# Performance work log

Hardware: AMD Instinct MI355X
Metric: run time of the kernel (lower is better)

Reference implementation:

```python
import jax, jax.numpy as jnp
import numpy as np

B, H, V, L, M, D, C = 64, 512, 50000, 400, 128, 64, 64
HC = 2 * D + M + 4  # controller LSTM hidden size (one head)
EPS = 1e-8


def _lstm_step(x, h, c, Wih, Whh, bih, bhh):
    g = x @ Wih.T + bih + h @ Whh.T + bhh
    i, f, gg, o = jnp.split(g, 4, axis=-1)
    c2 = jax.nn.sigmoid(f) * c + jax.nn.sigmoid(i) * jnp.tanh(gg)
    return jax.nn.sigmoid(o) * jnp.tanh(c2), c2


def _head_params(hc):
    # slices exactly as in LSTMMemoryController (k=0, single head)
    keys = hc[:, :M]                               # [B, M]
    kstr = jnp.exp(hc[:, D:D + 1])                 # [B, 1]
    gate = jax.nn.sigmoid(hc[:, D + 1:D + 2])      # [B, 1]
    erase = jax.nn.sigmoid(hc[:, D + 4:M + D + 4]) # [B, M]
    add = jax.nn.sigmoid(hc[:, 2 * D + 4:M + 2 * D + 4])  # [B, M]
    return keys, kstr, gate, erase, add


def _addressing(keys, kstr, gate, heads, memory):
    # torch cosine_similarity(keys.unsqueeze(2), memory, dim=2):
    # keys [B,M] broadcast along memory_dim D
    num = keys * memory.sum(-1)                                   # [B, M]
    nk = jnp.maximum(jnp.abs(keys) * jnp.sqrt(jnp.float32(D)), EPS)
    nm = jnp.maximum(jnp.linalg.norm(memory, axis=-1), EPS)
    cos = num / (nk * nm)
    content = jax.nn.softmax(kstr * cos, axis=1)                  # [B, M]
    # faithful to original: heads[k] indexes axis 0 (k=0) -> shape [1, M]
    gated = gate * content + (1.0 - gate) * heads[0]
    return gated[:, None, :]                                      # [B, 1, M]


def reference(input_ids, h0, c0, encoder_outputs, word_occurrence_indicator,
              coverage, memory, read_heads, write_heads,
              read_h, read_c, write_h, write_c,
              emb, attn_W, attn_b, cov_W, state_W, comb_W, comb_b,
              rpre_W, rpre_b, wpre_W, wpre_b,
              r_Wih, r_Whh, r_bih, r_bhh,
              w_Wih, w_Whh, w_bih, w_bhh,
              l_Wih, l_Whh, l_bih, l_bhh,
              out_W, out_b):
    embedded = emb[input_ids]                                     # [B, H]
    ia = jnp.concatenate([embedded, h0], 1) @ attn_W.T + attn_b  # [B, L]
    tc = (coverage + ia) @ cov_W.T
    ts = c0 @ state_W.T
    aw = jax.nn.softmax(tc + ia + ts, axis=1)                     # [B, L]
    attn_applied = jnp.einsum('bl,blh->bh', aw, encoder_outputs)  # [B, H]
    out0 = jnp.concatenate([embedded, attn_applied], 1) @ comb_W.T + comb_b  # [B, H]

    hm = jnp.concatenate([h0, memory.reshape(-1, M * D)], 1)
    rh, rc = _lstm_step(hm @ rpre_W.T + rpre_b, read_h, read_c, r_Wih, r_Whh, r_bih, r_bhh)
    wh, wc = _lstm_step(hm @ wpre_W.T + wpre_b, write_h, write_c, w_Wih, w_Whh, w_bih, w_bhh)
    rk, rks, rg, _, _ = _head_params(rh)
    wk, wks, wg, we, wa = _head_params(wh)
    rw = _addressing(rk, rks, rg, read_heads, memory)             # [B, 1, M]
    ww = _addressing(wk, wks, wg, write_heads, memory)            # [B, 1, M]

    read_in = jnp.einsum('bkm,bmd->bkd', rw, memory).reshape(-1, D)
    h1, c1 = _lstm_step(jnp.concatenate([out0, read_in], 1), h0, c0,
                        l_Wih, l_Whh, l_bih, l_bhh)
    # residual (h1 + out0) is computed in the original but unused by its output path

    w0 = ww[:, 0, :, None]                                        # [B, M, 1]
    new_memory = memory * (1.0 - w0 * we[:, :, None]) + w0 * wa[:, :, None]
    new_coverage = coverage + ia

    log_probs = jax.nn.log_softmax(c1[:, None, :] @ out_W.T + out_b, axis=-1)  # [B, 1, V]
    return log_probs, h1, c1, new_memory, new_coverage


def setup_inputs() -> dict:
    key = jax.random.key(0)
    ks = iter(jax.random.split(key, 48))

    def rn(shape, fan_in):
        return jax.random.normal(next(ks), shape, jnp.float32) / np.sqrt(fan_in)

    inp = {
        'input_ids': jax.random.randint(next(ks), (B,), 0, V),
        'h0': jax.random.normal(next(ks), (B, H), jnp.float32),
        'c0': jax.random.normal(next(ks), (B, H), jnp.float32),
        'encoder_outputs': jax.random.normal(next(ks), (B, L, H), jnp.float32),
        'word_occurrence_indicator': jnp.zeros((B, L), jnp.float32),
        'coverage': jnp.zeros((B, L), jnp.float32),
        'memory': jax.random.normal(next(ks), (B, M, D), jnp.float32),
        'read_heads': jnp.zeros((B, 1, M), jnp.float32),
        'write_heads': jnp.zeros((B, 1, M), jnp.float32),
        'read_h': jnp.zeros((B, HC), jnp.float32),
        'read_c': jnp.zeros((B, HC), jnp.float32),
        'write_h': jnp.zeros((B, HC), jnp.float32),
        'write_c': jnp.zeros((B, HC), jnp.float32),
        'emb': rn((V, H), H),
        'attn_W': rn((L, 2 * H), 2 * H), 'attn_b': jnp.zeros((L,), jnp.float32),
        'cov_W': rn((L, L), L),
        'state_W': rn((L, H), H),
        'comb_W': rn((H, 2 * H), 2 * H), 'comb_b': jnp.zeros((H,), jnp.float32),
        'rpre_W': rn((C, M * D + H), M * D + H), 'rpre_b': jnp.zeros((C,), jnp.float32),
        'wpre_W': rn((C, M * D + H), M * D + H), 'wpre_b': jnp.zeros((C,), jnp.float32),
        'r_Wih': rn((4 * HC, C), C), 'r_Whh': rn((4 * HC, HC), HC),
        'r_bih': jnp.zeros((4 * HC,), jnp.float32), 'r_bhh': jnp.zeros((4 * HC,), jnp.float32),
        'w_Wih': rn((4 * HC, C), C), 'w_Whh': rn((4 * HC, HC), HC),
        'w_bih': jnp.zeros((4 * HC,), jnp.float32), 'w_bhh': jnp.zeros((4 * HC,), jnp.float32),
        'l_Wih': rn((4 * H, H + D), H + D), 'l_Whh': rn((4 * H, H), H),
        'l_bih': jnp.zeros((4 * H,), jnp.float32), 'l_bhh': jnp.zeros((4 * H,), jnp.float32),
        'out_W': rn((V, H), H), 'out_b': jnp.zeros((V,), jnp.float32),
    }
    return inp
```

## Files before the change

### kernel.cpp

```cpp
#include <hip/hip_runtime.h>
#include <math.h>

#define BB 64
#define HH 512
#define VV 50000
#define LL 400
#define MM 128
#define DD 64
#define HC 260
#define EPSF 1e-8f

__device__ __forceinline__ float sigmoidf(float x){ return 1.0f/(1.0f+expf(-x)); }
__device__ __forceinline__ float wave_max(float v){
  #pragma unroll
  for(int o=32;o;o>>=1) v = fmaxf(v, __shfl_xor(v,o));
  return v;
}
__device__ __forceinline__ float wave_sum(float v){
  #pragma unroll
  for(int o=32;o;o>>=1) v += __shfl_xor(v,o);
  return v;
}

__global__ void k_embed(const int* __restrict__ ids, const float* __restrict__ emb,
                        const float* __restrict__ h0, float* __restrict__ xcat1,
                        float* __restrict__ xcat2){
  int idx = blockIdx.x*256 + threadIdx.x;
  if (idx >= BB*HH) return;
  int b = idx >> 9, h = idx & 511;
  float e = emb[(long)ids[b]*HH + h];
  xcat1[b*1024 + h] = e;
  xcat2[b*1024 + h] = e;
  xcat1[b*1024 + 512 + h] = h0[idx];
}

template<int NB, int FUSE>
__global__ __launch_bounds__(256) void k_gemv(const float* __restrict__ A,
                                              const float* __restrict__ A2,
                                              const float* __restrict__ W,
                                              const float* __restrict__ b1,
                                              float* __restrict__ C,
                                              int K, int N, int ldc){
  int b = blockIdx.y;
  int wid = threadIdx.x >> 6, lane = threadIdx.x & 63;
  int n = blockIdx.x*4 + wid;
  if (n >= N) return;
  const float4* A4  = (const float4*)(A + (long)b*K);
  const float4* A24 = (const float4*)(A2 + (long)b*K);
  const float4* W4  = (const float4*)(W + (long)n*K);
  int K4 = K >> 2;
  float acc = 0.f;
  for (int k = lane; k < K4; k += 64){
    float4 a = A4[k];
    if (FUSE){ float4 a2 = A24[k]; a.x+=a2.x; a.y+=a2.y; a.z+=a2.z; a.w+=a2.w; }
    float4 w = W4[k];
    acc += a.x*w.x + a.y*w.y + a.z*w.z + a.w*w.w;
  }
  acc = wave_sum(acc);
  if (lane == 0){
    if (NB) acc += b1[n];
    C[(long)b*ldc + n] = acc;
  }
}

__global__ void k_cov(const float* __restrict__ cov, const float* __restrict__ ia,
                      float* __restrict__ out){
  int idx = blockIdx.x*256 + threadIdx.x;
  if (idx >= BB*LL) return;
  out[idx] = cov[idx] + ia[idx];
}

__global__ __launch_bounds__(256) void k_softmax_aw(const float* __restrict__ ia,
                                                    const float* __restrict__ ts,
                                                    const float* __restrict__ tc,
                                                    float* __restrict__ aw){
  int b = blockIdx.x, t = threadIdx.x;
  int i0 = t, i1 = t + 256;
  float x0 = ia[b*LL+i0] + ts[b*LL+i0] + tc[b*LL+i0];
  float x1 = (i1 < LL) ? (ia[b*LL+i1] + ts[b*LL+i1] + tc[b*LL+i1]) : -INFINITY;
  __shared__ float sm[4], ss[4];
  float m = wave_max(fmaxf(x0, x1));
  if ((t & 63) == 0) sm[t>>6] = m;
  __syncthreads();
  m = fmaxf(fmaxf(sm[0], sm[1]), fmaxf(sm[2], sm[3]));
  float e0 = expf(x0 - m);
  float e1 = (i1 < LL) ? expf(x1 - m) : 0.0f;
  float s = wave_sum(e0 + e1);
  if ((t & 63) == 0) ss[t>>6] = s;
  __syncthreads();
  float tot = ss[0] + ss[1] + ss[2] + ss[3];
  float inv = 1.0f / tot;
  aw[b*LL + i0] = e0 * inv;
  if (i1 < LL) aw[b*LL + i1] = e1 * inv;
}

__global__ __launch_bounds__(256) void k_attn_part(const float* __restrict__ aw,
                                                   const float* __restrict__ enc,
                                                   float* __restrict__ part){
  int b = blockIdx.x, lc = blockIdx.y, t = threadIdx.x;
  const float* awb = aw + b*LL + lc*25;
  const float* eb  = enc + ((long)b*LL + lc*25)*HH;
  float a0 = 0.f, a1 = 0.f;
  for (int l = 0; l < 25; l++){
    float a = awb[l];
    a0 += a * eb[(long)l*HH + t];
    a1 += a * eb[(long)l*HH + t + 256];
  }
  part[((b*16 + lc) << 9) + t]       = a0;
  part[((b*16 + lc) << 9) + t + 256] = a1;
}

__global__ void k_attn_reduce(const float* __restrict__ part, float* __restrict__ xcat2){
  int idx = blockIdx.x*256 + threadIdx.x;
  if (idx >= BB*HH) return;
  int b = idx >> 9, h = idx & 511;
  float s = 0.f;
  #pragma unroll
  for (int lc = 0; lc < 16; lc++) s += part[((b*16 + lc) << 9) + h];
  xcat2[b*1024 + 512 + h] = s;
}

__global__ __launch_bounds__(256) void k_pre_partial(const float* __restrict__ h0,
                                                     const float* __restrict__ mem,
                                                     const float* __restrict__ rW,
                                                     const float* __restrict__ wW,
                                                     float* __restrict__ part){
  int c = blockIdx.x;
  int which = blockIdx.y;
  const float* W = which ? wW : rW;
  __shared__ __align__(16) float As[32][68];
  __shared__ __align__(16) float Ws[32][68];
  int tid = threadIdx.x;
  int kk = tid & 31, r0 = tid >> 5;
  int tn = (tid & 15)*4, tb = (tid >> 4)*4;
  float acc[4][4] = {};
  for (int s = 0; s < 4; s++){
    int kg = c*128 + s*32 + kk;
    #pragma unroll
    for (int i = 0; i < 8; i++){
      int b = r0 + i*8;
      As[kk][b] = (kg < 512) ? h0[b*HH + kg] : mem[(long)b*8192 + (kg - 512)];
      Ws[kk][r0 + i*8] = W[(long)(r0 + i*8)*8704 + kg];
    }
    __syncthreads();
    #pragma unroll
    for (int k = 0; k < 32; k++){
      float4 a4 = *(const float4*)&As[k][tb];
      float4 w4 = *(const float4*)&Ws[k][tn];
      acc[0][0] += a4.x*w4.x; acc[0][1] += a4.x*w4.y; acc[0][2] += a4.x*w4.z; acc[0][3] += a4.x*w4.w;
      acc[1][0] += a4.y*w4.x; acc[1][1] += a4.y*w4.y; acc[1][2] += a4.y*w4.z; acc[1][3] += a4.y*w4.w;
      acc[2][0] += a4.z*w4.x; acc[2][1] += a4.z*w4.y; acc[2][2] += a4.z*w4.z; acc[2][3] += a4.z*w4.w;
      acc[3][0] += a4.w*w4.x; acc[3][1] += a4.w*w4.y; acc[3][2] += a4.w*w4.z; acc[3][3] += a4.w*w4.w;
    }
    __syncthreads();
  }
  float* p = part + ((long)which*68 + c)*4096;
  #pragma unroll
  for (int i = 0; i < 4; i++)
    #pragma unroll
    for (int j = 0; j < 4; j++)
      p[(tb + i)*64 + tn + j] = acc[i][j];
}

__global__ void k_pre_reduce(const float* __restrict__ part, const float* __restrict__ rb,
                             const float* __restrict__ wb, float* __restrict__ pre_r,
                             float* __restrict__ pre_w){
  int idx = blockIdx.x*256 + threadIdx.x;
  if (idx >= 8192) return;
  int which = idx >> 12;
  int bj = idx & 4095;
  const float* p = part + (long)which*68*4096 + bj;
  float s = 0.f;
  #pragma unroll
  for (int c = 0; c < 68; c++) s += p[c*4096];
  int j = bj & 63;
  s += which ? wb[j] : rb[j];
  (which ? pre_w : pre_r)[bj] = s;
}

__global__ __launch_bounds__(256) void k_gates_rw(const float* __restrict__ pre_r,
    const float* __restrict__ pre_w, const float* __restrict__ read_h,
    const float* __restrict__ write_h,
    const float* __restrict__ rWih, const float* __restrict__ rWhh,
    const float* __restrict__ rbih, const float* __restrict__ rbhh,
    const float* __restrict__ wWih, const float* __restrict__ wWhh,
    const float* __restrict__ wbih, const float* __restrict__ wbhh,
    float* __restrict__ g_r, float* __restrict__ g_w){
  int which = blockIdx.z;
  int b = blockIdx.y;
  int wid = threadIdx.x >> 6, lane = threadIdx.x & 63;
  int n = blockIdx.x*4 + wid;
  const float* pre = which ? pre_w : pre_r;
  const float* hh  = which ? write_h : read_h;
  const float* Wih = which ? wWih : rWih;
  const float* Whh = which ? wWhh : rWhh;
  float acc = pre[b*64 + lane] * Wih[n*64 + lane];
  const float* hb = hh + b*HC;
  const float* wr = Whh + (long)n*HC;
  #pragma unroll
  for (int i = 0; i < 5; i++){
    int k = lane + i*64;
    if (k < HC) acc += hb[k]*wr[k];
  }
  acc = wave_sum(acc);
  if (lane == 0){
    acc += (which ? wbih : rbih)[n] + (which ? wbhh : rbhh)[n];
    (which ? g_w : g_r)[(long)b*4*HC + n] = acc;
  }
}

__global__ void k_lstm_rw(const float* __restrict__ g_r, const float* __restrict__ g_w,
                          const float* __restrict__ read_c, const float* __restrict__ write_c,
                          float* __restrict__ rh, float* __restrict__ wh){
  int idx = blockIdx.x*256 + threadIdx.x;
  if (idx >= 2*BB*HC) return;
  int which = idx >= BB*HC;
  int r = which ? idx - BB*HC : idx;
  int b = r / HC, j = r - b*HC;
  const float* g = (which ? g_w : g_r) + (long)b*4*HC;
  float c2 = sigmoidf(g[HC + j]) * (which ? write_c : read_c)[r]
           + sigmoidf(g[j]) * tanhf(g[2*HC + j]);
  (which ? wh : rh)[r] = sigmoidf(g[3*HC + j]) * tanhf(c2);
}

__global__ __launch_bounds__(128) void k_address(const float* __restrict__ rh,
                                                 const float* __restrict__ whv,
                                                 const float* __restrict__ rheads,
                                                 const float* __restrict__ wheads,
                                                 const float* __restrict__ mem,
                                                 float* __restrict__ rwout,
                                                 float* __restrict__ wwout){
  int which = blockIdx.y;
  int b = blockIdx.x, m = threadIdx.x;
  const float* hc = which ? whv : rh;
  const float* heads0 = which ? wheads : rheads;
  float* wout = which ? wwout : rwout;
  const float* mr = mem + ((long)b*MM + m)*DD;
  float s = 0.f, q = 0.f;
  #pragma unroll 8
  for (int d = 0; d < DD; d++){ float v = mr[d]; s += v; q += v*v; }
  float key  = hc[b*HC + m];
  float kstr = expf(hc[b*HC + 64]);
  float gate = sigmoidf(hc[b*HC + 65]);
  float nk = fmaxf(fabsf(key)*8.0f, EPSF);
  float nm = fmaxf(sqrtf(q), EPSF);
  float z  = kstr * (key*s) / (nk*nm);
  __shared__ float sm[2], ss[2];
  float mx = wave_max(z);
  if ((m & 63) == 0) sm[m>>6] = mx;
  __syncthreads();
  mx = fmaxf(sm[0], sm[1]);
  float e = expf(z - mx);
  float w = wave_sum(e);
  if ((m & 63) == 0) ss[m>>6] = w;
  __syncthreads();
  float content = e / (ss[0] + ss[1]);
  wout[b*MM + m] = gate*content + (1.0f - gate)*heads0[m];
}

__global__ void k_readin(const float* __restrict__ rw, const float* __restrict__ mem,
                         float* __restrict__ xcat3){
  int b = blockIdx.x, d = threadIdx.x;
  float s = 0.f;
  for (int m = 0; m < MM; m++) s += rw[b*MM + m] * mem[((long)b*MM + m)*DD + d];
  xcat3[b*576 + 512 + d] = s;
}

__global__ void k_newmem(const float* __restrict__ mem, const float* __restrict__ ww,
                         const float* __restrict__ wh, float* __restrict__ out){
  int idx = blockIdx.x*256 + threadIdx.x;
  if (idx >= BB*MM*DD) return;
  int b = idx >> 13;
  int m = (idx & 8191) >> 6;
  float w0 = ww[b*MM + m];
  float we = sigmoidf(wh[b*HC + 68 + m]);
  float wa = sigmoidf(wh[b*HC + 132 + m]);
  out[idx] = mem[idx]*(1.0f - w0*we) + w0*wa;
}

__global__ __launch_bounds__(256) void k_lgates_part(const float* __restrict__ xcat3,
                                                     const float* __restrict__ h0,
                                                     const float* __restrict__ lWih,
                                                     const float* __restrict__ lWhh,
                                                     float* __restrict__ part){
  int s = blockIdx.y;
  int n0 = blockIdx.x*64;
  const float *A, *W; int lda, k0, nchunk;
  if (s < 2){ A = xcat3; W = lWih; lda = 576; k0 = s*288; nchunk = 9; }
  else      { A = h0;    W = lWhh; lda = 512; k0 = (s-2)*256; nchunk = 8; }
  __shared__ __align__(16) float As[32][68];
  __shared__ __align__(16) float Ws[32][68];
  int tid = threadIdx.x;
  int kk = tid & 31, r0 = tid >> 5;
  int tn = (tid & 15)*4, tb = (tid >> 4)*4;
  float acc[4][4] = {};
  for (int sc = 0; sc < nchunk; sc++){
    int kg = k0 + sc*32 + kk;
    #pragma unroll
    for (int i = 0; i < 8; i++){
      int r = r0 + i*8;
      As[kk][r] = A[(long)r*lda + kg];
      Ws[kk][r] = W[(long)(n0 + r)*lda + kg];
    }
    __syncthreads();
    #pragma unroll
    for (int k = 0; k < 32; k++){
      float4 a4 = *(const float4*)&As[k][tb];
      float4 w4 = *(const float4*)&Ws[k][tn];
      acc[0][0] += a4.x*w4.x; acc[0][1] += a4.x*w4.y; acc[0][2] += a4.x*w4.z; acc[0][3] += a4.x*w4.w;
      acc[1][0] += a4.y*w4.x; acc[1][1] += a4.y*w4.y; acc[1][2] += a4.y*w4.z; acc[1][3] += a4.y*w4.w;
      acc[2][0] += a4.z*w4.x; acc[2][1] += a4.z*w4.y; acc[2][2] += a4.z*w4.z; acc[2][3] += a4.z*w4.w;
      acc[3][0] += a4.w*w4.x; acc[3][1] += a4.w*w4.y; acc[3][2] += a4.w*w4.z; acc[3][3] += a4.w*w4.w;
    }
    __syncthreads();
  }
  float* p = part + (long)s*BB*2048;
  #pragma unroll
  for (int i = 0; i < 4; i++)
    #pragma unroll
    for (int j = 0; j < 4; j++)
      p[(long)(tb + i)*2048 + n0 + tn + j] = acc[i][j];
}

__global__ void k_lstm_l(const float* __restrict__ part, const float* __restrict__ bih,
                         const float* __restrict__ bhh, const float* __restrict__ c0,
                         float* __restrict__ h1, float* __restrict__ c1){
  int idx = blockIdx.x*256 + threadIdx.x;
  if (idx >= BB*HH) return;
  int b = idx >> 9, j = idx & 511;
  float gv[4];
  #pragma unroll
  for (int gi = 0; gi < 4; gi++){
    int n = gi*512 + j;
    float s = bih[n] + bhh[n];
    #pragma unroll
    for (int sp = 0; sp < 4; sp++) s += part[(long)sp*BB*2048 + (long)b*2048 + n];
    gv[gi] = s;
  }
  float c2 = sigmoidf(gv[1])*c0[idx] + sigmoidf(gv[0])*tanhf(gv[2]);
  h1[idx] = sigmoidf(gv[3])*tanhf(c2);
  c1[idx] = c2;
}

__global__ __launch_bounds__(256) void k_gemm_logits(const float* __restrict__ A,
                                                     const float* __restrict__ W,
                                                     const float* __restrict__ bias,
                                                     float* __restrict__ C){
  __shared__ __align__(16) float As[32][68];
  __shared__ __align__(16) float Ws[32][68];
  int tid = threadIdx.x;
  int n0  = blockIdx.x * 64;
  int tn  = (tid & 15) * 4;
  int tb  = (tid >> 4) * 4;
  int kk  = tid & 31;
  int r0  = tid >> 5;
  float acc[4][4] = {};
  for (int k0 = 0; k0 < HH; k0 += 32){
    int kg = k0 + kk;
    #pragma unroll
    for (int i = 0; i < 8; i++){
      int b = r0 + i*8;
      As[kk][b] = A[(long)b*HH + kg];
      int n = n0 + r0 + i*8;
      Ws[kk][r0 + i*8] = (n < VV) ? W[(long)n*HH + kg] : 0.0f;
    }
    __syncthreads();
    #pragma unroll
    for (int k = 0; k < 32; k++){
      float4 a4 = *(const float4*)&As[k][tb];
      float4 w4 = *(const float4*)&Ws[k][tn];
      acc[0][0] += a4.x*w4.x; acc[0][1] += a4.x*w4.y; acc[0][2] += a4.x*w4.z; acc[0][3] += a4.x*w4.w;
      acc[1][0] += a4.y*w4.x; acc[1][1] += a4.y*w4.y; acc[1][2] += a4.y*w4.z; acc[1][3] += a4.y*w4.w;
      acc[2][0] += a4.z*w4.x; acc[2][1] += a4.z*w4.y; acc[2][2] += a4.z*w4.z; acc[2][3] += a4.z*w4.w;
      acc[3][0] += a4.w*w4.x; acc[3][1] += a4.w*w4.y; acc[3][2] += a4.w*w4.z; acc[3][3] += a4.w*w4.w;
    }
    __syncthreads();
  }
  #pragma unroll
  for (int i = 0; i < 4; i++){
    #pragma unroll
    for (int j = 0; j < 4; j++){
      int n = n0 + tn + j;
      if (n < VV) C[(long)(tb + i)*VV + n] = acc[i][j] + bias[n];
    }
  }
}

__global__ __launch_bounds__(256) void k_ls1(const float* __restrict__ lp,
                                             float* __restrict__ pm, float* __restrict__ ps){
  int b = blockIdx.y, c = blockIdx.x, t = threadIdx.x;
  const float* row = lp + (long)b*VV + c*2000;
  float mx = -INFINITY;
  for (int i = t; i < 2000; i += 256) mx = fmaxf(mx, row[i]);
  __shared__ float sm[4], ss[4];
  mx = wave_max(mx);
  if ((t & 63) == 0) sm[t>>6] = mx;
  __syncthreads();
  mx = fmaxf(fmaxf(sm[0], sm[1]), fmaxf(sm[2], sm[3]));
  float s = 0.f;
  for (int i = t; i < 2000; i += 256) s += expf(row[i] - mx);
  s = wave_sum(s);
  if ((t & 63) == 0) ss[t>>6] = s;
  __syncthreads();
  if (t == 0){ pm[b*25 + c] = mx; ps[b*25 + c] = ss[0]+ss[1]+ss[2]+ss[3]; }
}

__global__ void k_ls2(const float* __restrict__ pm, const float* __restrict__ ps,
                      float* __restrict__ lse){
  int b = threadIdx.x;
  float m = -INFINITY;
  for (int c = 0; c < 25; c++) m = fmaxf(m, pm[b*25 + c]);
  float s = 0.f;
  for (int c = 0; c < 25; c++) s += ps[b*25 + c]*expf(pm[b*25 + c] - m);
  lse[b] = m + logf(s);
}

__global__ void k_ls3(float* __restrict__ lp, const float* __restrict__ lse){
  int idx = blockIdx.x*256 + threadIdx.x;
  if (idx >= BB*VV) return;
  int b = idx / VV;
  lp[idx] -= lse[b];
}

extern "C" void kernel_launch(void* const* d_in, const int* in_sizes, int n_in,
                              void* d_out, int out_size, void* d_ws, size_t ws_size,
                              hipStream_t stream) {
  const int*   ids     = (const int*)  d_in[0];
  const float* h0      = (const float*)d_in[1];
  const float* c0      = (const float*)d_in[2];
  const float* enc     = (const float*)d_in[3];
  const float* cov     = (const float*)d_in[5];
  const float* mem     = (const float*)d_in[6];
  const float* rheads  = (const float*)d_in[7];
  const float* wheads  = (const float*)d_in[8];
  const float* read_h  = (const float*)d_in[9];
  const float* read_c  = (const float*)d_in[10];
  const float* write_h = (const float*)d_in[11];
  const float* write_c = (const float*)d_in[12];
  const float* emb     = (const float*)d_in[13];
  const float* attn_W  = (const float*)d_in[14];
  const float* attn_b  = (const float*)d_in[15];
  const float* cov_W   = (const float*)d_in[16];
  const float* state_W = (const float*)d_in[17];
  const float* comb_W  = (const float*)d_in[18];
  const float* comb_b  = (const float*)d_in[19];
  const float* rpre_W  = (const float*)d_in[20];
  const float* rpre_b  = (const float*)d_in[21];
  const float* wpre_W  = (const float*)d_in[22];
  const float* wpre_b  = (const float*)d_in[23];
  const float* r_Wih   = (const float*)d_in[24];
  const float* r_Whh   = (const float*)d_in[25];
  const float* r_bih   = (const float*)d_in[26];
  const float* r_bhh   = (const float*)d_in[27];
  const float* w_Wih   = (const float*)d_in[28];
  const float* w_Whh   = (const float*)d_in[29];
  const float* w_bih   = (const float*)d_in[30];
  const float* w_bhh   = (const float*)d_in[31];
  const float* l_Wih   = (const float*)d_in[32];
  const float* l_Whh   = (const float*)d_in[33];
  const float* l_bih   = (const float*)d_in[34];
  const float* l_bhh   = (const float*)d_in[35];
  const float* out_W   = (const float*)d_in[36];
  const float* out_b   = (const float*)d_in[37];

  float* out  = (float*)d_out;
  float* lp   = out;
  float* h1   = out + 3200000;
  float* c1   = h1 + 32768;
  float* nmem = c1 + 32768;
  float* ncov = nmem + 524288;

  float* w = (float*)d_ws;
  float* xcat1 = w;
  float* xcat2 = xcat1 + 65536;
  float* xcat3 = xcat2 + 65536;
  float* ia    = xcat3 + 36864;
  float* ts    = ia + 25600;
  float* tc    = ts + 25600;
  float* aw    = tc + 25600;
  float* U     = aw + 25600;
  float* pre_r = U + 557056;
  float* pre_w = pre_r + 4096;
  float* g_r   = pre_w + 4096;
  float* g_w   = g_r + 66560;
  float* rh    = g_w + 66560;
  float* wh    = rh + 16640;
  float* rw    = wh + 16640;
  float* wwgt  = rw + 8192;
  float* pm    = wwgt + 8192;
  float* ps    = pm + 1600;
  float* lse   = ps + 1600;

  k_embed<<<128, 256, 0, stream>>>(ids, emb, h0, xcat1, xcat2);
  k_gemv<1,0><<<dim3(100,64), 256, 0, stream>>>(xcat1, xcat1, attn_W, attn_b, ia, 1024, LL, LL);
  k_gemv<0,0><<<dim3(100,64), 256, 0, stream>>>(c0, c0, state_W, nullptr, ts, HH, LL, LL);
  k_cov<<<100, 256, 0, stream>>>(cov, ia, ncov);
  k_gemv<0,1><<<dim3(100,64), 256, 0, stream>>>(cov, ia, cov_W, nullptr, tc, LL, LL, LL);
  k_softmax_aw<<<64, 256, 0, stream>>>(ia, ts, tc, aw);
  k_attn_part<<<dim3(64,16), 256, 0, stream>>>(aw, enc, U);
  k_attn_reduce<<<128, 256, 0, stream>>>(U, xcat2);
  k_gemv<1,0><<<dim3(128,64), 256, 0, stream>>>(xcat2, xcat2, comb_W, comb_b, xcat3, 1024, HH, 576);

  k_pre_partial<<<dim3(68,2), 256, 0, stream>>>(h0, mem, rpre_W, wpre_W, U);
  k_pre_reduce<<<32, 256, 0, stream>>>(U, rpre_b, wpre_b, pre_r, pre_w);

  k_gates_rw<<<dim3(260,64,2), 256, 0, stream>>>(pre_r, pre_w, read_h, write_h,
      r_Wih, r_Whh, r_bih, r_bhh, w_Wih, w_Whh, w_bih, w_bhh, g_r, g_w);
  k_lstm_rw<<<130, 256, 0, stream>>>(g_r, g_w, read_c, write_c, rh, wh);

  k_address<<<dim3(64,2), 128, 0, stream>>>(rh, wh, rheads, wheads, mem, rw, wwgt);
  k_readin<<<64, 64, 0, stream>>>(rw, mem, xcat3);
  k_newmem<<<2048, 256, 0, stream>>>(mem, wwgt, wh, nmem);

  k_lgates_part<<<dim3(32,4), 256, 0, stream>>>(xcat3, h0, l_Wih, l_Whh, U);
  k_lstm_l<<<128, 256, 0, stream>>>(U, l_bih, l_bhh, c0, h1, c1);

  k_gemm_logits<<<782, 256, 0, stream>>>(c1, out_W, out_b, lp);
  k_ls1<<<dim3(25,64), 256, 0, stream>>>(lp, pm, ps);
  k_ls2<<<1, 64, 0, stream>>>(pm, ps, lse);
  k_ls3<<<12500, 256, 0, stream>>>(lp, lse);
}
```

Before: 559.9 us.

## Use bf16 MFMA for logits, wave-GEMV for pre-projection, fuse LSTM gates

The vocabulary logits GEMM now runs on bf16 MFMA instructions, converting out_W to bf16 on the fly and taking c1 from a bf16 copy written by the LSTM kernel. The read/write pre-projection changes from a 68-chunk tiled GEMM to a per-wave float4 GEMV split into 8 K-chunks, which shrinks the reduction. The LSTM gate matmul and the cell update are fused into one wave-per-output kernel, removing the partial buffer and one launch. Rounding the logits inputs to bf16 lowers precision, and the GEMV forms re-read the small activations once per output row.

```diff
diff --git a/kernel.cpp b/kernel.cpp
--- a/kernel.cpp
+++ b/kernel.cpp
@@ -10,7 +10,14 @@
 #define HC 260
 #define EPSF 1e-8f
 
+typedef __attribute__((ext_vector_type(8))) short bf16x8;
+typedef __attribute__((ext_vector_type(4))) float f32x4;
+
 __device__ __forceinline__ float sigmoidf(float x){ return 1.0f/(1.0f+expf(-x)); }
+__device__ __forceinline__ unsigned short bf16_rne(float f){
+  unsigned u = __float_as_uint(f);
+  return (unsigned short)((u + 0x7fffu + ((u >> 16) & 1u)) >> 16);
+}
 __device__ __forceinline__ float wave_max(float v){
   #pragma unroll
   for(int o=32;o;o>>=1) v = fmaxf(v, __shfl_xor(v,o));
@@ -120,46 +127,33 @@
   xcat2[b*1024 + 512 + h] = s;
 }
 
-__global__ __launch_bounds__(256) void k_pre_partial(const float* __restrict__ h0,
-                                                     const float* __restrict__ mem,
-                                                     const float* __restrict__ rW,
-                                                     const float* __restrict__ wW,
-                                                     float* __restrict__ part){
-  int c = blockIdx.x;
-  int which = blockIdx.y;
+__global__ __launch_bounds__(256) void k_pre_gemv(const float* __restrict__ h0,
+                                                  const float* __restrict__ mem,
+                                                  const float* __restrict__ rW,
+                                                  const float* __restrict__ wW,
+                                                  float* __restrict__ part){
+  int wid = threadIdx.x >> 6, lane = threadIdx.x & 63;
+  int n = blockIdx.x*4 + wid;
+  int b = blockIdx.y;
+  int z = blockIdx.z;
+  int which = z >> 3, chunk = z & 7;
   const float* W = which ? wW : rW;
-  __shared__ __align__(16) float As[32][68];
-  __shared__ __align__(16) float Ws[32][68];
-  int tid = threadIdx.x;
-  int kk = tid & 31, r0 = tid >> 5;
-  int tn = (tid & 15)*4, tb = (tid >> 4)*4;
-  float acc[4][4] = {};
-  for (int s = 0; s < 4; s++){
-    int kg = c*128 + s*32 + kk;
-    #pragma unroll
-    for (int i = 0; i < 8; i++){
-      int b = r0 + i*8;
-      As[kk][b] = (kg < 512) ? h0[b*HH + kg] : mem[(long)b*8192 + (kg - 512)];
-      Ws[kk][r0 + i*8] = W[(long)(r0 + i*8)*8704 + kg];
+  const float4* W4 = (const float4*)(W + (long)n*8704 + chunk*1088);
+  const float4* H4 = (const float4*)(h0 + (long)b*HH);
+  const float4* M4 = (const float4*)(mem + (long)b*8192 + (chunk*1088 - 512));
+  float acc = 0.f;
+  #pragma unroll
+  for (int i = 0; i < 5; i++){
+    int k4 = lane + i*64;
+    if (k4 < 272){
+      int kg4 = chunk*272 + k4;
+      float4 a = (kg4 < 128) ? H4[kg4] : M4[k4];
+      float4 w = W4[k4];
+      acc += a.x*w.x + a.y*w.y + a.z*w.z + a.w*w.w;
     }
-    __syncthreads();
-    #pragma unroll
-    for (int k = 0; k < 32; k++){
-      float4 a4 = *(const float4*)&As[k][tb];
-      float4 w4 = *(const float4*)&Ws[k][tn];
-      acc[0][0] += a4.x*w4.x; acc[0][1] += a4.x*w4.y; acc[0][2] += a4.x*w4.z; acc[0][3] += a4.x*w4.w;
-      acc[1][0] += a4.y*w4.x; acc[1][1] += a4.y*w4.y; acc[1][2] += a4.y*w4.z; acc[1][3] += a4.y*w4.w;
-      acc[2][0] += a4.z*w4.x; acc[2][1] += a4.z*w4.y; acc[2][2] += a4.z*w4.z; acc[2][3] += a4.z*w4.w;
-      acc[3][0] += a4.w*w4.x; acc[3][1] += a4.w*w4.y; acc[3][2] += a4.w*w4.z; acc[3][3] += a4.w*w4.w;
-    }
-    __syncthreads();
-  }
-  float* p = part + ((long)which*68 + c)*4096;
-  #pragma unroll
-  for (int i = 0; i < 4; i++)
-    #pragma unroll
-    for (int j = 0; j < 4; j++)
-      p[(tb + i)*64 + tn + j] = acc[i][j];
+  }
+  acc = wave_sum(acc);
+  if (lane == 0) part[z*4096 + b*64 + n] = acc;
 }
 
 __global__ void k_pre_reduce(const float* __restrict__ part, const float* __restrict__ rb,
@@ -168,14 +162,13 @@
   int idx = blockIdx.x*256 + threadIdx.x;
   if (idx >= 8192) return;
   int which = idx >> 12;
-  int bj = idx & 4095;
-  const float* p = part + (long)which*68*4096 + bj;
+  int r = idx & 4095;
   float s = 0.f;
   #pragma unroll
-  for (int c = 0; c < 68; c++) s += p[c*4096];
-  int j = bj & 63;
-  s += which ? wb[j] : rb[j];
-  (which ? pre_w : pre_r)[bj] = s;
+  for (int c = 0; c < 8; c++) s += part[((which<<3)+c)*4096 + r];
+  int n = r & 63;
+  s += which ? wb[n] : rb[n];
+  (which ? pre_w : pre_r)[r] = s;
 }
 
 __global__ __launch_bounds__(256) void k_gates_rw(const float* __restrict__ pre_r,
@@ -278,111 +271,93 @@
   out[idx] = mem[idx]*(1.0f - w0*we) + w0*wa;
 }
 
-__global__ __launch_bounds__(256) void k_lgates_part(const float* __restrict__ xcat3,
-                                                     const float* __restrict__ h0,
-                                                     const float* __restrict__ lWih,
-                                                     const float* __restrict__ lWhh,
-                                                     float* __restrict__ part){
-  int s = blockIdx.y;
-  int n0 = blockIdx.x*64;
-  const float *A, *W; int lda, k0, nchunk;
-  if (s < 2){ A = xcat3; W = lWih; lda = 576; k0 = s*288; nchunk = 9; }
-  else      { A = h0;    W = lWhh; lda = 512; k0 = (s-2)*256; nchunk = 8; }
-  __shared__ __align__(16) float As[32][68];
-  __shared__ __align__(16) float Ws[32][68];
-  int tid = threadIdx.x;
-  int kk = tid & 31, r0 = tid >> 5;
-  int tn = (tid & 15)*4, tb = (tid >> 4)*4;
-  float acc[4][4] = {};
-  for (int sc = 0; sc < nchunk; sc++){
-    int kg = k0 + sc*32 + kk;
+__global__ __launch_bounds__(256) void k_lstm_main(const float* __restrict__ xcat3,
+                                                   const float* __restrict__ h0,
+                                                   const float* __restrict__ lWih,
+                                                   const float* __restrict__ lWhh,
+                                                   const float* __restrict__ bih,
+                                                   const float* __restrict__ bhh,
+                                                   const float* __restrict__ c0,
+                                                   float* __restrict__ h1,
+                                                   float* __restrict__ c1,
+                                                   unsigned short* __restrict__ c1b){
+  int wid = threadIdx.x >> 6, lane = threadIdx.x & 63;
+  int j = blockIdx.x*4 + wid;
+  int b = blockIdx.y;
+  const float4* A1 = (const float4*)(xcat3 + (long)b*576);
+  const float4* A2 = (const float4*)(h0 + (long)b*HH);
+  float gv[4];
+  #pragma unroll
+  for (int g = 0; g < 4; g++){
+    int n = g*HH + j;
+    const float4* W1 = (const float4*)(lWih + (long)n*576);
+    const float4* W2 = (const float4*)(lWhh + (long)n*HH);
+    float s = 0.f;
     #pragma unroll
-    for (int i = 0; i < 8; i++){
-      int r = r0 + i*8;
-      As[kk][r] = A[(long)r*lda + kg];
-      Ws[kk][r] = W[(long)(n0 + r)*lda + kg];
+    for (int i = 0; i < 3; i++){
+      int k = lane + i*64;
+      if (k < 144){ float4 a = A1[k], w = W1[k]; s += a.x*w.x + a.y*w.y + a.z*w.z + a.w*w.w; }
     }
-    __syncthreads();
     #pragma unroll
-    for (int k = 0; k < 32; k++){
-      float4 a4 = *(const float4*)&As[k][tb];
-      float4 w4 = *(const float4*)&Ws[k][tn];
-      acc[0][0] += a4.x*w4.x; acc[0][1] += a4.x*w4.y; acc[0][2] += a4.x*w4.z; acc[0][3] += a4.x*w4.w;
-      acc[1][0] += a4.y*w4.x; acc[1][1] += a4.y*w4.y; acc[1][2] += a4.y*w4.z; acc[1][3] += a4.y*w4.w;
-      acc[2][0] += a4.z*w4.x; acc[2][1] += a4.z*w4.y; acc[2][2] += a4.z*w4.z; acc[2][3] += a4.z*w4.w;
-      acc[3][0] += a4.w*w4.x; acc[3][1] += a4.w*w4.y; acc[3][2] += a4.w*w4.z; acc[3][3] += a4.w*w4.w;
+    for (int i = 0; i < 2; i++){
+      int k = lane + i*64;
+      float4 a = A2[k], w = W2[k]; s += a.x*w.x + a.y*w.y + a.z*w.z + a.w*w.w;
     }
-    __syncthreads();
-  }
-  float* p = part + (long)s*BB*2048;
-  #pragma unroll
-  for (int i = 0; i < 4; i++)
+    gv[g] = wave_sum(s);
+  }
+  if (lane == 0){
     #pragma unroll
-    for (int j = 0; j < 4; j++)
-      p[(long)(tb + i)*2048 + n0 + tn + j] = acc[i][j];
-}
-
-__global__ void k_lstm_l(const float* __restrict__ part, const float* __restrict__ bih,
-                         const float* __restrict__ bhh, const float* __restrict__ c0,
-                         float* __restrict__ h1, float* __restrict__ c1){
-  int idx = blockIdx.x*256 + threadIdx.x;
-  if (idx >= BB*HH) return;
-  int b = idx >> 9, j = idx & 511;
-  float gv[4];
-  #pragma unroll
-  for (int gi = 0; gi < 4; gi++){
-    int n = gi*512 + j;
-    float s = bih[n] + bhh[n];
-    #pragma unroll
-    for (int sp = 0; sp < 4; sp++) s += part[(long)sp*BB*2048 + (long)b*2048 + n];
-    gv[gi] = s;
-  }
-  float c2 = sigmoidf(gv[1])*c0[idx] + sigmoidf(gv[0])*tanhf(gv[2]);
-  h1[idx] = sigmoidf(gv[3])*tanhf(c2);
-  c1[idx] = c2;
-}
-
-__global__ __launch_bounds__(256) void k_gemm_logits(const float* __restrict__ A,
+    for (int g = 0; g < 4; g++){ int n = g*HH + j; gv[g] += bih[n] + bhh[n]; }
+    float c2 = sigmoidf(gv[1])*c0[b*HH + j] + sigmoidf(gv[0])*tanhf(gv[2]);
+    h1[b*HH + j] = sigmoidf(gv[3])*tanhf(c2);
+    c1[b*HH + j] = c2;
+    c1b[b*HH + j] = bf16_rne(c2);
+  }
+}
+
+__global__ __launch_bounds__(256) void k_logits_mfma(const unsigned short* __restrict__ Ab,
                                                      const float* __restrict__ W,
                                                      const float* __restrict__ bias,
                                                      float* __restrict__ C){
-  __shared__ __align__(16) float As[32][68];
-  __shared__ __align__(16) float Ws[32][68];
-  int tid = threadIdx.x;
-  int n0  = blockIdx.x * 64;
-  int tn  = (tid & 15) * 4;
-  int tb  = (tid >> 4) * 4;
-  int kk  = tid & 31;
-  int r0  = tid >> 5;
-  float acc[4][4] = {};
-  for (int k0 = 0; k0 < HH; k0 += 32){
-    int kg = k0 + kk;
-    #pragma unroll
-    for (int i = 0; i < 8; i++){
-      int b = r0 + i*8;
-      As[kk][b] = A[(long)b*HH + kg];
-      int n = n0 + r0 + i*8;
-      Ws[kk][r0 + i*8] = (n < VV) ? W[(long)n*HH + kg] : 0.0f;
-    }
-    __syncthreads();
-    #pragma unroll
-    for (int k = 0; k < 32; k++){
-      float4 a4 = *(const float4*)&As[k][tb];
-      float4 w4 = *(const float4*)&Ws[k][tn];
-      acc[0][0] += a4.x*w4.x; acc[0][1] += a4.x*w4.y; acc[0][2] += a4.x*w4.z; acc[0][3] += a4.x*w4.w;
-      acc[1][0] += a4.y*w4.x; acc[1][1] += a4.y*w4.y; acc[1][2] += a4.y*w4.z; acc[1][3] += a4.y*w4.w;
-      acc[2][0] += a4.z*w4.x; acc[2][1] += a4.z*w4.y; acc[2][2] += a4.z*w4.z; acc[2][3] += a4.z*w4.w;
-      acc[3][0] += a4.w*w4.x; acc[3][1] += a4.w*w4.y; acc[3][2] += a4.w*w4.z; acc[3][3] += a4.w*w4.w;
-    }
-    __syncthreads();
-  }
-  #pragma unroll
-  for (int i = 0; i < 4; i++){
-    #pragma unroll
-    for (int j = 0; j < 4; j++){
-      int n = n0 + tn + j;
-      if (n < VV) C[(long)(tb + i)*VV + n] = acc[i][j] + bias[n];
-    }
+  int wid = threadIdx.x >> 6, lane = threadIdx.x & 63;
+  int strip = blockIdx.x*4 + wid;
+  if (strip >= 3125) return;
+  int nl = lane & 15;
+  int q  = lane >> 4;
+  int n  = strip*16 + nl;
+  const float* wrow = W + (long)n*HH + q*8;
+  const unsigned short* a0p = Ab + (0*16 + nl)*HH + q*8;
+  const unsigned short* a1p = Ab + (1*16 + nl)*HH + q*8;
+  const unsigned short* a2p = Ab + (2*16 + nl)*HH + q*8;
+  const unsigned short* a3p = Ab + (3*16 + nl)*HH + q*8;
+  f32x4 acc0 = {0.f,0.f,0.f,0.f}, acc1 = acc0, acc2 = acc0, acc3 = acc0;
+  #pragma unroll 4
+  for (int ks = 0; ks < 16; ks++){
+    const float4* wp = (const float4*)(wrow + ks*32);
+    float4 w0 = wp[0];
+    float4 w1 = wp[1];
+    bf16x8 bf;
+    bf[0] = (short)bf16_rne(w0.x); bf[1] = (short)bf16_rne(w0.y);
+    bf[2] = (short)bf16_rne(w0.z); bf[3] = (short)bf16_rne(w0.w);
+    bf[4] = (short)bf16_rne(w1.x); bf[5] = (short)bf16_rne(w1.y);
+    bf[6] = (short)bf16_rne(w1.z); bf[7] = (short)bf16_rne(w1.w);
+    bf16x8 a0 = *(const bf16x8*)(a0p + ks*32);
+    bf16x8 a1 = *(const bf16x8*)(a1p + ks*32);
+    bf16x8 a2 = *(const bf16x8*)(a2p + ks*32);
+    bf16x8 a3 = *(const bf16x8*)(a3p + ks*32);
+    acc0 = __builtin_amdgcn_mfma_f32_16x16x32_bf16(a0, bf, acc0, 0, 0, 0);
+    acc1 = __builtin_amdgcn_mfma_f32_16x16x32_bf16(a1, bf, acc1, 0, 0, 0);
+    acc2 = __builtin_amdgcn_mfma_f32_16x16x32_bf16(a2, bf, acc2, 0, 0, 0);
+    acc3 = __builtin_amdgcn_mfma_f32_16x16x32_bf16(a3, bf, acc3, 0, 0, 0);
+  }
+  float bv = bias[n];
+  #pragma unroll
+  for (int r = 0; r < 4; r++){
+    int m = q*4 + r;
+    C[(long)(m     )*VV + n] = acc0[r] + bv;
+    C[(long)(m + 16)*VV + n] = acc1[r] + bv;
+    C[(long)(m + 32)*VV + n] = acc2[r] + bv;
+    C[(long)(m + 48)*VV + n] = acc3[r] + bv;
   }
 }
 
@@ -490,6 +465,7 @@
   float* pm    = wwgt + 8192;
   float* ps    = pm + 1600;
   float* lse   = ps + 1600;
+  unsigned short* c1b = (unsigned short*)(lse + 64);
 
   k_embed<<<128, 256, 0, stream>>>(ids, emb, h0, xcat1, xcat2);
   k_gemv<1,0><<<dim3(100,64), 256, 0, stream>>>(xcat1, xcat1, attn_W, attn_b, ia, 1024, LL, LL);
@@ -501,7 +477,7 @@
   k_attn_reduce<<<128, 256, 0, stream>>>(U, xcat2);
   k_gemv<1,0><<<dim3(128,64), 256, 0, stream>>>(xcat2, xcat2, comb_W, comb_b, xcat3, 1024, HH, 576);
 
-  k_pre_partial<<<dim3(68,2), 256, 0, stream>>>(h0, mem, rpre_W, wpre_W, U);
+  k_pre_gemv<<<dim3(16,64,16), 256, 0, stream>>>(h0, mem, rpre_W, wpre_W, U);
   k_pre_reduce<<<32, 256, 0, stream>>>(U, rpre_b, wpre_b, pre_r, pre_w);
 
   k_gates_rw<<<dim3(260,64,2), 256, 0, stream>>>(pre_r, pre_w, read_h, write_h,
@@ -512,10 +488,10 @@
   k_readin<<<64, 64, 0, stream>>>(rw, mem, xcat3);
   k_newmem<<<2048, 256, 0, stream>>>(mem, wwgt, wh, nmem);
 
-  k_lgates_part<<<dim3(32,4), 256, 0, stream>>>(xcat3, h0, l_Wih, l_Whh, U);
-  k_lstm_l<<<128, 256, 0, stream>>>(U, l_bih, l_bhh, c0, h1, c1);
-
-  k_gemm_logits<<<782, 256, 0, stream>>>(c1, out_W, out_b, lp);
+  k_lstm_main<<<dim3(128,64), 256, 0, stream>>>(xcat3, h0, l_Wih, l_Whh, l_bih, l_bhh,
+                                                c0, h1, c1, c1b);
+
+  k_logits_mfma<<<782, 256, 0, stream>>>(c1b, out_W, out_b, lp);
   k_ls1<<<dim3(25,64), 256, 0, stream>>>(lp, pm, ps);
   k_ls2<<<1, 64, 0, stream>>>(pm, ps, lse);
   k_ls3<<<12500, 256, 0, stream>>>(lp, lse);
```

New measurement: 503.7 us. 10.0% less time.
